# Kernel tuning notes

Measured on AMD Instinct MI355X. Metric: run time of the kernel, lower is better.

## Reference

```python
import jax, jax.numpy as jnp
import numpy as np
import math

B, S, D, H = 8, 1024, 512, 8
DH = D // H
SCALE_BASE = 512


def _xpos(x, downscale):
    # x: [B, H, S, DH]; xpos rotary with exponential scale (jamie-stirling RetNet impl)
    s = x.shape[-2]
    d = x.shape[-1]
    half = d // 2
    sv = (jnp.arange(0, d, 2, dtype=jnp.float32) + 0.4 * d) / (1.4 * d)      # [half]
    power = jnp.arange(s, dtype=jnp.float32) / SCALE_BASE
    scale = sv[None, :] ** power[:, None]                                     # [s, half]
    inv_freq = 1.0 / (10000.0 ** (jnp.arange(half, dtype=jnp.float32) / half))
    ang = jnp.arange(s, dtype=jnp.float32)[:, None] * inv_freq[None, :]       # [s, half]
    if downscale:
        scale = 1.0 / scale
    sin = jnp.repeat(jnp.sin(ang) * scale, 2, axis=-1)                        # [s, d]
    cos = jnp.repeat(jnp.cos(ang) * scale, 2, axis=-1)
    rot = jnp.stack((-x[..., 1::2], x[..., ::2]), axis=-1).reshape(x.shape)   # rotate_every_two
    return x * cos + rot * sin


def setup_inputs() -> dict:
    key = jax.random.key(0)
    ks = jax.random.split(key, 7)
    X = jax.random.normal(ks[0], (B, S, D), dtype=jnp.float32)
    # per-head projections stacked: torch init randn/hidden_size
    W_Q = jax.random.normal(ks[1], (H, D, DH), dtype=jnp.float32) / D
    W_K = jax.random.normal(ks[2], (H, D, DH), dtype=jnp.float32) / D
    W_V = jax.random.normal(ks[3], (H, D, DH), dtype=jnp.float32) / D
    W_G = jax.random.normal(ks[4], (D, D), dtype=jnp.float32) / D
    W_O = jax.random.normal(ks[5], (D, D), dtype=jnp.float32) / D
    gn_weight = jnp.ones((D,), dtype=jnp.float32)
    gn_bias = jnp.zeros((D,), dtype=jnp.float32)
    return {"X": X, "W_Q": W_Q, "W_K": W_K, "W_V": W_V, "W_G": W_G,
            "W_O": W_O, "gn_weight": gn_weight, "gn_bias": gn_bias}


def reference(X, W_Q, W_K, W_V, W_G, W_O, gn_weight, gn_bias):
    b, s, _ = X.shape
    # per-head decay gammas and symmetric (non-causal) decay matrix D
    gammas = 1.0 - jnp.exp(jnp.linspace(math.log(1.0 / 32), math.log(1.0 / 512), H)).astype(jnp.float32)
    n = jnp.arange(s)
    Dmat = gammas[:, None, None] ** jnp.abs(n[:, None] - n[None, :]).astype(jnp.float32)  # [H,s,s]
    Q = _xpos(jnp.einsum('bsd,hde->bhse', X, W_Q), False)
    K = _xpos(jnp.einsum('bsd,hde->bhse', X, W_K), True)
    V = jnp.einsum('bsd,hde->bhse', X, W_V)
    scores = jnp.einsum('bhse,bhte->bhst', Q, K)
    p = jax.nn.softmax(scores, axis=-1) * Dmat[None]          # decay-weighted softmax
    Y = jnp.einsum('bhst,bhte->bhse', p, V)                    # [b,H,s,DH]
    Y = jnp.moveaxis(Y, 1, 2).reshape(b, s, H * DH)            # concat heads -> [b,s,D]
    # GroupNorm(H groups) over flattened rows [b*s, D]
    Yg = Y.reshape(-1, H, DH)
    mu = Yg.mean(axis=-1, keepdims=True)
    var = Yg.var(axis=-1, keepdims=True)
    Yn = ((Yg - mu) * jax.lax.rsqrt(var + 1e-5)).reshape(-1, H * DH)
    Yn = (Yn * gn_weight + gn_bias).reshape(b, s, H * DH)
    G = X @ W_G
    swish = G * jax.nn.sigmoid(G)
    return (swish * Yn) @ W_O
```

## Files before the change

kernel.cpp:

```cpp
#include <hip/hip_runtime.h>
#include <math.h>

#define B_ 8
#define S_ 1024
#define D_ 512
#define H_ 8
#define DH_ 64
#define M_ (B_*S_)

typedef __attribute__((ext_vector_type(8))) short short8;
typedef __attribute__((ext_vector_type(4))) short s16x4;
typedef __attribute__((ext_vector_type(4))) float f32x4;
typedef __attribute__((ext_vector_type(4))) unsigned int u32x4;

__device__ inline void tsplit(float x, short& hs, short& ls) {
  unsigned u = __float_as_uint(x);
  hs = (short)(u >> 16);
  float r = x - __uint_as_float(u & 0xFFFF0000u);
  ls = (short)(__float_as_uint(r) >> 16);
}
__device__ inline void splitpack(f32x4 a, f32x4 b, short8& hh, short8& ll) {
  union { u32x4 u; short8 s; } H, L;
#pragma unroll
  for (int j = 0; j < 2; ++j) {
    unsigned u0 = __float_as_uint(a[2 * j]);
    unsigned u1 = __float_as_uint(a[2 * j + 1]);
    H.u[j] = (u0 >> 16) | (u1 & 0xFFFF0000u);
    float r0 = a[2 * j]     - __uint_as_float(u0 & 0xFFFF0000u);
    float r1 = a[2 * j + 1] - __uint_as_float(u1 & 0xFFFF0000u);
    L.u[j] = (__float_as_uint(r0) >> 16) | (__float_as_uint(r1) & 0xFFFF0000u);
    unsigned v0 = __float_as_uint(b[2 * j]);
    unsigned v1 = __float_as_uint(b[2 * j + 1]);
    H.u[2 + j] = (v0 >> 16) | (v1 & 0xFFFF0000u);
    float s0 = b[2 * j]     - __uint_as_float(v0 & 0xFFFF0000u);
    float s1 = b[2 * j + 1] - __uint_as_float(v1 & 0xFFFF0000u);
    L.u[2 + j] = (__float_as_uint(s0) >> 16) | (__float_as_uint(s1) & 0xFFFF0000u);
  }
  hh = H.s; ll = L.s;
}
__device__ inline f32x4 mfma16(short8 a, short8 b, f32x4 c) {
  return __builtin_amdgcn_mfma_f32_16x16x32_bf16(a, b, c, 0, 0, 0);
}
__device__ inline void gload_lds16(const void* g, void* l) {
  __builtin_amdgcn_global_load_lds(
      (const __attribute__((address_space(1))) void*)g,
      (__attribute__((address_space(3))) void*)l, 16, 0, 0);
}


__global__ void xpos_table_kernel(float* __restrict__ tab) {
  int idx = blockIdx.x * 256 + threadIdx.x;
  int s = idx >> 5, i = idx & 31;
  float sv = (2.0f * (float)i + 0.4f * 64.0f) / (1.4f * 64.0f);
  float p = (float)s / 512.0f;
  float scale = powf(sv, p);
  float inv_freq = powf(10000.0f, -((float)i / 32.0f));
  float ang = (float)s * inv_freq;
  float sn = sinf(ang), cs = cosf(ang);
  tab[idx]          = cs * scale;
  tab[32768 + idx]  = sn * scale;
  tab[65536 + idx]  = cs / scale;
  tab[98304 + idx]  = sn / scale;
}

__global__ __launch_bounds__(256) void xsplit_kernel(
    const float* __restrict__ X, short* __restrict__ Xh, short* __restrict__ Xl) {
  const int tid = threadIdx.x;
  const size_t tile = ((size_t)blockIdx.x * 16 + blockIdx.y) * 4096;
#pragma unroll
  for (int i = 0; i < 2; ++i) {
    int idx = tid + i * 256;
    int g = idx >> 6, sl = idx & 63;
    int m = blockIdx.x * 128 + g * 16 + (sl & 15);
    int k = blockIdx.y * 32 + (sl >> 4) * 8;
    const float* xp = X + (size_t)m * 512 + k;
    f32x4 a = *(const f32x4*)xp;
    f32x4 b = *(const f32x4*)(xp + 4);
    short8 hh, ll;
    splitpack(a, b, hh, ll);
    *(short8*)(Xh + tile + (size_t)idx * 8) = hh;
    *(short8*)(Xl + tile + (size_t)idx * 8) = ll;
  }
}

__global__ __launch_bounds__(256) void wprep_kernel(
    const float* __restrict__ Wq, const float* __restrict__ Wk,
    const float* __restrict__ Wv, const float* __restrict__ Wg,
    short* __restrict__ BTh, short* __restrict__ BTl, int gonly) {
  __shared__ float t[64][65];
  const int n0 = blockIdx.x * 64, k0 = blockIdx.y * 64;
  const int tid = threadIdx.x;
  const float* src;
  int ld;
  if (gonly) {
    src = Wg + (size_t)k0 * 512 + n0; ld = 512;
  } else {
    int w = n0 >> 9, nn = n0 & 511;
    if (w == 3) { src = Wg + (size_t)k0 * 512 + nn; ld = 512; }
    else {
      const float* W = (w == 0) ? Wq : ((w == 1) ? Wk : Wv);
      int h = nn >> 6;
      src = W + (size_t)h * D_ * DH_ + (size_t)k0 * 64; ld = 64;
    }
  }
#pragma unroll
  for (int i = 0; i < 4; ++i) {
    int idx = tid + i * 256;
    int kk = idx >> 4, nl4 = (idx & 15) * 4;
    float4 v = *(const float4*)(src + (size_t)kk * ld + nl4);
    t[kk][nl4] = v.x; t[kk][nl4 + 1] = v.y; t[kk][nl4 + 2] = v.z; t[kk][nl4 + 3] = v.w;
  }
  __syncthreads();
#pragma unroll
  for (int i = 0; i < 2; ++i) {
    int idx = tid + i * 256;
    int nl = idx >> 3, ck = idx & 7;
    short8 hh, ll;
#pragma unroll
    for (int j = 0; j < 8; ++j) {
      short h_, l_;
      tsplit(t[ck * 8 + j][nl], h_, l_);
      hh[j] = h_; ll[j] = l_;
    }
    const int n = n0 + nl, k = k0 + ck * 8;
    const size_t off = ((size_t)((n >> 7) * 16 + (k >> 5))) * 4096
                     + (size_t)((n >> 4) & 7) * 512
                     + (size_t)(((k >> 3) & 3) * 16 + (n & 15)) * 8;
    *(short8*)(BTh + off) = hh;
    *(short8*)(BTl + off) = ll;
  }
}

template<int NSUB, int FUSED>
__global__ __launch_bounds__(256, 2) void gemm_mfma_kernel(
    const short* __restrict__ Ah, const short* __restrict__ Al,
    const short* __restrict__ BTh, const short* __restrict__ BTl,
    const float* __restrict__ tab,
    short* __restrict__ QhO, short* __restrict__ QlO,
    short* __restrict__ KhO, short* __restrict__ KlO,
    short* __restrict__ VhT, short* __restrict__ VlT,
    float* __restrict__ G) {
  constexpr int NT = NSUB * 32;
  constexpr int BSZ = NT * 32;
  __shared__ __align__(16) short AsH[2 * 4096], AsL[2 * 4096];
  __shared__ __align__(16) short BsH[2 * BSZ], BsL[2 * BSZ];
  const int m0 = blockIdx.x * 128, by = blockIdx.y;
  const int tid = threadIdx.x, w = tid >> 6, lane = tid & 63;
  const int lx = lane & 15, quad = lane >> 4;
  const int wr = w >> 1, wc = w & 1;
  f32x4 acc[4][NSUB] = {};

  auto stage = [&](int bsel, int kt) {
    const size_t ta = ((size_t)blockIdx.x * 16 + kt) * 4096 + lane * 8;
    gload_lds16(Ah + ta + (size_t)w * 512,       &AsH[bsel * 4096 + w * 512]);
    gload_lds16(Ah + ta + (size_t)(w + 4) * 512, &AsH[bsel * 4096 + (w + 4) * 512]);
    gload_lds16(Al + ta + (size_t)w * 512,       &AsL[bsel * 4096 + w * 512]);
    gload_lds16(Al + ta + (size_t)(w + 4) * 512, &AsL[bsel * 4096 + (w + 4) * 512]);
    if constexpr (NSUB == 4) {
      const size_t tb = ((size_t)by * 16 + kt) * 4096 + lane * 8;
      gload_lds16(BTh + tb + (size_t)w * 512,       &BsH[bsel * BSZ + w * 512]);
      gload_lds16(BTh + tb + (size_t)(w + 4) * 512, &BsH[bsel * BSZ + (w + 4) * 512]);
      gload_lds16(BTl + tb + (size_t)w * 512,       &BsL[bsel * BSZ + w * 512]);
      gload_lds16(BTl + tb + (size_t)(w + 4) * 512, &BsL[bsel * BSZ + (w + 4) * 512]);
    } else {
      const size_t tb = ((size_t)(by >> 1) * 16 + kt) * 4096
                      + (size_t)(by & 1) * 2048 + lane * 8;
      const short* src = (w < 2) ? BTh : BTl;
      short* dst = (w < 2) ? &BsH[bsel * BSZ] : &BsL[bsel * BSZ];
      const int wq = (w & 1) * 2;
      gload_lds16(src + tb + (size_t)wq * 512,       dst + wq * 512);
      gload_lds16(src + tb + (size_t)(wq + 1) * 512, dst + (wq + 1) * 512);
    }
  };

  stage(0, 0);
  int cur = 0;
  for (int t = 0; t < 16; ++t) {
    asm volatile("s_waitcnt lgkmcnt(0)" ::: "memory");
    __builtin_amdgcn_s_barrier();
    asm volatile("" ::: "memory");
    if (t < 15) {
      stage(cur ^ 1, t + 1);
      if constexpr (NSUB == 4)
        asm volatile("s_waitcnt vmcnt(12)" ::: "memory");
      else
        asm volatile("s_waitcnt vmcnt(6)" ::: "memory");
    } else {
      asm volatile("s_waitcnt vmcnt(0)" ::: "memory");
    }
    __builtin_amdgcn_s_barrier();
    asm volatile("" ::: "memory");

    short8 fah[4], fal[4], fbh[NSUB], fbl[NSUB];
#pragma unroll
    for (int i = 0; i < 4; ++i) {
      fah[i] = *(const short8*)&AsH[cur * 4096 + (wr * 4 + i) * 512 + lane * 8];
      fal[i] = *(const short8*)&AsL[cur * 4096 + (wr * 4 + i) * 512 + lane * 8];
    }
#pragma unroll
    for (int i = 0; i < NSUB; ++i) {
      const int g = (NSUB == 4 ? wc * 4 : wc * 2) + i;
      fbh[i] = *(const short8*)&BsH[cur * BSZ + g * 512 + lane * 8];
      fbl[i] = *(const short8*)&BsL[cur * BSZ + g * 512 + lane * 8];
    }
#pragma unroll
    for (int ms = 0; ms < 4; ++ms)
#pragma unroll
      for (int ns = 0; ns < NSUB; ++ns) {
        f32x4 a = acc[ms][ns];
        a = mfma16(fah[ms], fbh[ns], a);
        a = mfma16(fal[ms], fbh[ns], a);
        a = mfma16(fah[ms], fbl[ns], a);
        acc[ms][ns] = a;
      }
    cur ^= 1;
  }
  if constexpr (FUSED) {
    const int w4 = by >> 2;
    const int ncb = (by & 3) * 128 + wc * 64;
    if (w4 < 2) {
      short* Ph = (w4 == 0) ? QhO : KhO;
      short* Pl = (w4 == 0) ? QlO : KlO;
      const float* ct = tab + (w4 ? 65536 : 0);
      const float* st = tab + (w4 ? 98304 : 32768);
#pragma unroll
      for (int ms = 0; ms < 4; ++ms) {
        const int m = m0 + wr * 64 + ms * 16 + quad * 4;
        const int b = m >> 10, sbase = m & 1023;
#pragma unroll
        for (int ns = 0; ns < 4; ++ns) {
          const int n = ncb + ns * 16 + lx;
          const int h = n >> 6, e = n & 63;
          const int i0 = e >> 1;
          const float sgn = (e & 1) ? 1.0f : -1.0f;
          short* ph = Ph + (((size_t)(b * 8 + h)) * 1024 + sbase) * 64 + e;
          short* pl = Pl + (((size_t)(b * 8 + h)) * 1024 + sbase) * 64 + e;
#pragma unroll
          for (int rg = 0; rg < 4; ++rg) {
            const int s = sbase + rg;
            float v = acc[ms][ns][rg];
            float vp = __shfl_xor(v, 1);
            float o = v * ct[s * 32 + i0] + sgn * vp * st[s * 32 + i0];
            short h_, l_;
            tsplit(o, h_, l_);
            ph[rg * 64] = h_;
            pl[rg * 64] = l_;
          }
        }
      }
    } else if (w4 == 2) {
#pragma unroll
      for (int ms = 0; ms < 4; ++ms) {
        const int m = m0 + wr * 64 + ms * 16 + quad * 4;
        const int b = m >> 10, s = m & 1023;
#pragma unroll
        for (int ns = 0; ns < 4; ++ns) {
          const int n = ncb + ns * 16 + lx;
          const int h = n >> 6, e = n & 63;
          s16x4 hh, ll;
#pragma unroll
          for (int rg = 0; rg < 4; ++rg) {
            short h_, l_;
            tsplit(acc[ms][ns][rg], h_, l_);
            hh[rg] = h_; ll[rg] = l_;
          }
          size_t off = (((size_t)(b * 8 + h)) * 64 + e) * 1024 + s;
          *(s16x4*)(VhT + off) = hh;
          *(s16x4*)(VlT + off) = ll;
        }
      }
    } else {
#pragma unroll
      for (int ms = 0; ms < 4; ++ms) {
        const int m = m0 + wr * 64 + ms * 16 + quad * 4;
#pragma unroll
        for (int ns = 0; ns < 4; ++ns) {
          const int n = ncb + ns * 16 + lx;
#pragma unroll
          for (int rg = 0; rg < 4; ++rg) G[(size_t)(m + rg) * 512 + n] = acc[ms][ns][rg];
        }
      }
    }
  } else {
#pragma unroll
    for (int ms = 0; ms < 4; ++ms) {
      const int m = m0 + wr * 64 + ms * 16 + quad * 4;
#pragma unroll
      for (int ns = 0; ns < NSUB; ++ns) {
        const int n = by * NT + wc * (NSUB * 16) + ns * 16 + lx;
#pragma unroll
        for (int rg = 0; rg < 4; ++rg) G[(size_t)(m + rg) * 512 + n] = acc[ms][ns][rg];
      }
    }
  }
}

__global__ __launch_bounds__(256, 2) void attn_mfma_kernel(
    const short* __restrict__ Qh, const short* __restrict__ Ql,
    const short* __restrict__ Kh, const short* __restrict__ Kl,
    const short* __restrict__ VhT, const short* __restrict__ VlT,
    const float* __restrict__ Gp,
    const float* __restrict__ gnw, const float* __restrict__ gnb,
    short* __restrict__ Zh, short* __restrict__ Zl) {
  __shared__ __align__(16) short KhS[4096];
  __shared__ __align__(16) short KlS[4096];
  __shared__ __align__(16) short VhS[4096];
  __shared__ __align__(16) short VlS[4096];
  __shared__ __align__(16) short PhS[4][2048];
  const int bh = blockIdx.x, s0 = blockIdx.y * 128;
  const int b = bh >> 3, h = bh & 7;
  const int tid = threadIdx.x;
  const int w = tid >> 6, lane = tid & 63;
  const int lx = lane & 15, quad = lane >> 4;
  const int s0w = s0 + w * 32;
  const float l0c = -3.4657359027997265f;
  const float l1c = -6.2383246250395075f;
  const float gamma = 1.0f - expf(l0c + (float)h * (l1c - l0c) / 7.0f);
  const float lg2g = log2f(gamma);
  const short* Qbh = Qh + (size_t)bh * S_ * DH_;
  const short* Qbl = Ql + (size_t)bh * S_ * DH_;
  const short* Kbh = Kh + (size_t)bh * S_ * DH_;
  const short* Kbl = Kl + (size_t)bh * S_ * DH_;
  const short* VbH = VhT + (size_t)bh * DH_ * S_;
  const short* VbL = VlT + (size_t)bh * DH_ * S_;

  float cl[4], cr[4], w4g[4], b4g[4];
#pragma unroll
  for (int ns = 0; ns < 4; ++ns) {
    cl[ns] = exp2f(lg2g * (float)(ns * 16 + lx));
    cr[ns] = exp2f(lg2g * (float)(63 - ns * 16 - lx));
    w4g[ns] = gnw[h * DH_ + ns * 16 + lx];
    b4g[ns] = gnb[h * DH_ + ns * 16 + lx];
  }

  short8 qfh[2][2], qfl[2][2];
#pragma unroll
  for (int ms = 0; ms < 2; ++ms)
#pragma unroll
    for (int kc = 0; kc < 2; ++kc) {
      size_t off = (size_t)(s0w + ms * 16 + lx) * DH_ + kc * 32 + quad * 8;
      qfh[ms][kc] = *(const short8*)(Qbh + off);
      qfl[ms][kc] = *(const short8*)(Qbl + off);
    }

  const int rA = tid >> 3, gsA = tid & 7;
  const int wA = gsA ^ (rA & 7);
  const int rB = rA + 32;
  short8 kAh, kAl, vAh, vAl, kBh, kBl, vBh, vBl;
#define ISSUE_KV(T0N) do {                                                   \
    kAh = *(const short8*)(Kbh + (size_t)((T0N) + rA) * 64 + gsA * 8);       \
    kAl = *(const short8*)(Kbl + (size_t)((T0N) + rA) * 64 + gsA * 8);       \
    vAh = *(const short8*)(VbH + (size_t)rA * 1024 + (T0N) + gsA * 8);       \
    vAl = *(const short8*)(VbL + (size_t)rA * 1024 + (T0N) + gsA * 8);       \
    kBh = *(const short8*)(Kbh + (size_t)((T0N) + rB) * 64 + gsA * 8);       \
    kBl = *(const short8*)(Kbl + (size_t)((T0N) + rB) * 64 + gsA * 8);       \
    vBh = *(const short8*)(VbH + (size_t)rB * 1024 + (T0N) + gsA * 8);       \
    vBl = *(const short8*)(VbL + (size_t)rB * 1024 + (T0N) + gsA * 8);       \
  } while (0)
#define WRITE_KV() do {                                                      \
    *(short8*)(KhS + rA * 64 + wA * 8) = kAh;                                \
    *(short8*)(KlS + rA * 64 + wA * 8) = kAl;                                \
    *(short8*)(VhS + rA * 64 + wA * 8) = vAh;                                \
    *(short8*)(VlS + rA * 64 + wA * 8) = vAl;                                \
    *(short8*)(KhS + rB * 64 + wA * 8) = kBh;                                \
    *(short8*)(KlS + rB * 64 + wA * 8) = kBl;                                \
    *(short8*)(VhS + rB * 64 + wA * 8) = vBh;                                \
    *(short8*)(VlS + rB * 64 + wA * 8) = vBl;                                \
  } while (0)

  f32x4 O[2][4] = {};
  float lsum[2][4] = {};

  ISSUE_KV(0);
  WRITE_KV();
  for (int t = 0; t < 16; ++t) {
    const int t0 = t * 64;
    __syncthreads();
    f32x4 acc[2][4];
#pragma unroll
    for (int ns = 0; ns < 4; ++ns) {
      const int rowk = ns * 16 + lx, rk = (rowk & 7) << 3;
      const short* Kc0 = &KhS[rowk * 64];
      const short* Kc1 = &KlS[rowk * 64];
      short8 kh0 = *(const short8*)(Kc0 + (((quad) << 3) ^ rk));
      short8 kh1 = *(const short8*)(Kc0 + (((4 | quad) << 3) ^ rk));
      short8 kl0 = *(const short8*)(Kc1 + (((quad) << 3) ^ rk));
      short8 kl1 = *(const short8*)(Kc1 + (((4 | quad) << 3) ^ rk));
#pragma unroll
      for (int ms = 0; ms < 2; ++ms) {
        f32x4 a = {};
        a = mfma16(qfh[ms][0], kh0, a);
        a = mfma16(qfl[ms][0], kh0, a);
        a = mfma16(qfh[ms][0], kl0, a);
        a = mfma16(qfh[ms][1], kh1, a);
        a = mfma16(qfl[ms][1], kh1, a);
        a = mfma16(qfh[ms][1], kl1, a);
        acc[ms][ns] = a;
      }
    }
    if (t < 15) ISSUE_KV(t0 + 64);
    const int cse = (t0 + 63 < s0w) ? 0 : ((t0 > s0w + 31) ? 1 : 2);
#pragma unroll
    for (int ms = 0; ms < 2; ++ms)
#pragma unroll
      for (int rg = 0; rg < 4; ++rg) {
        const int rloc = ms * 16 + quad * 4 + rg;
        const int srow = s0w + rloc;
        float pe[4], p[4];
#pragma unroll
        for (int ns = 0; ns < 4; ++ns) pe[ns] = __expf(acc[ms][ns][rg]);
        lsum[ms][rg] += (pe[0] + pe[1]) + (pe[2] + pe[3]);
        if (cse == 0) {
          float rf = exp2f(lg2g * (float)(srow - t0 - 63));
#pragma unroll
          for (int ns = 0; ns < 4; ++ns) p[ns] = pe[ns] * rf * cr[ns];
        } else if (cse == 1) {
          float rf = exp2f(lg2g * (float)(t0 - srow));
#pragma unroll
          for (int ns = 0; ns < 4; ++ns) p[ns] = pe[ns] * rf * cl[ns];
        } else {
#pragma unroll
          for (int ns = 0; ns < 4; ++ns)
            p[ns] = pe[ns] * exp2f(lg2g * fabsf((float)(srow - (t0 + ns * 16 + lx))));
        }
        const int r7s = rloc & 7;
        short* Pw = &PhS[w][rloc * 64 + (lx & 7)];
#pragma unroll
        for (int ns = 0; ns < 4; ++ns)
          Pw[(((ns * 2 + (lx >> 3)) ^ r7s) << 3)] =
              (short)((__float_as_uint(p[ns]) + 0x8000u) >> 16);
      }
    short8 pf[2][2];
#pragma unroll
    for (int ms = 0; ms < 2; ++ms) {
      const int rowp = ms * 16 + lx, rp = (rowp & 7) << 3;
#pragma unroll
      for (int kc = 0; kc < 2; ++kc)
        pf[ms][kc] = *(const short8*)&PhS[w][rowp * 64 + ((((kc * 4 + quad)) << 3) ^ rp)];
    }
#pragma unroll
    for (int ns = 0; ns < 4; ++ns) {
      const int rowv = ns * 16 + lx, rv = (rowv & 7) << 3;
      const short* Vc0 = &VhS[rowv * 64];
      const short* Vc1 = &VlS[rowv * 64];
      short8 vh0 = *(const short8*)(Vc0 + (((quad) << 3) ^ rv));
      short8 vh1 = *(const short8*)(Vc0 + (((4 | quad) << 3) ^ rv));
      short8 vl0 = *(const short8*)(Vc1 + (((quad) << 3) ^ rv));
      short8 vl1 = *(const short8*)(Vc1 + (((4 | quad) << 3) ^ rv));
#pragma unroll
      for (int ms = 0; ms < 2; ++ms) {
        f32x4 o = O[ms][ns];
        o = mfma16(pf[ms][0], vh0, o);
        o = mfma16(pf[ms][0], vl0, o);
        o = mfma16(pf[ms][1], vh1, o);
        o = mfma16(pf[ms][1], vl1, o);
        O[ms][ns] = o;
      }
    }
    __syncthreads();
    if (t < 15) WRITE_KV();
  }
#undef ISSUE_KV
#undef WRITE_KV
#pragma unroll
  for (int ms = 0; ms < 2; ++ms)
#pragma unroll
    for (int rg = 0; rg < 4; ++rg) {
      float s = lsum[ms][rg];
      s += __shfl_xor(s, 1);
      s += __shfl_xor(s, 2);
      s += __shfl_xor(s, 4);
      s += __shfl_xor(s, 8);
      const float inv = 1.0f / s;
      const int srow = s0w + ms * 16 + quad * 4 + rg;
      float y[4];
      float rs = 0.0f;
#pragma unroll
      for (int ns = 0; ns < 4; ++ns) { y[ns] = O[ms][ns][rg] * inv; rs += y[ns]; }
      rs += __shfl_xor(rs, 1);
      rs += __shfl_xor(rs, 2);
      rs += __shfl_xor(rs, 4);
      rs += __shfl_xor(rs, 8);
      const float mu = rs * (1.0f / 64.0f);
      float vv = 0.0f;
#pragma unroll
      for (int ns = 0; ns < 4; ++ns) { float d = y[ns] - mu; vv += d * d; }
      vv += __shfl_xor(vv, 1);
      vv += __shfl_xor(vv, 2);
      vv += __shfl_xor(vv, 4);
      vv += __shfl_xor(vv, 8);
      const float rstd = rsqrtf(vv * (1.0f / 64.0f) + 1e-5f);
      const size_t base = (size_t)(b * S_ + srow) * D_ + h * DH_;
      const int m = b * S_ + srow;
      const size_t zb = ((size_t)((m >> 7) * 16 + h * 2)) * 4096
                      + (size_t)((m >> 4) & 7) * 512 + (size_t)(m & 15) * 8;
#pragma unroll
      for (int ns = 0; ns < 4; ++ns) {
        float g = Gp[base + ns * 16 + lx];
        float sw = g / (1.0f + __expf(-g));
        float z = sw * ((y[ns] - mu) * rstd * w4g[ns] + b4g[ns]);
        short zh_, zl_;
        tsplit(z, zh_, zl_);
        const size_t off = zb + (size_t)(ns >> 1) * 4096
                         + (size_t)(((ns * 2 + (lx >> 3)) & 3) * 128) + (lx & 7);
        Zh[off] = zh_;
        Zl[off] = zl_;
      }
    }
}

extern "C" void kernel_launch(void* const* d_in, const int* in_sizes, int n_in,
                              void* d_out, int out_size, void* d_ws, size_t ws_size,
                              hipStream_t stream) {
  const float* X   = (const float*)d_in[0];
  const float* Wq  = (const float*)d_in[1];
  const float* Wk  = (const float*)d_in[2];
  const float* Wv  = (const float*)d_in[3];
  const float* Wg  = (const float*)d_in[4];
  const float* Wo  = (const float*)d_in[5];
  const float* gnw = (const float*)d_in[6];
  const float* gnb = (const float*)d_in[7];
  float* out = (float*)d_out;
  float* ws  = (float*)d_ws;
  const size_t NB = (size_t)M_ * D_;
  float* R0 = ws;
  float* R1 = ws + NB;
  float* R2 = ws + 2 * NB;
  float* R3 = ws + 3 * NB;
  float* tab = ws + 4 * NB;
  short* BTh = (short*)R3;
  short* BTl = BTh + (size_t)2048 * 512;
  short* Xh  = BTh + (size_t)2 * 2048 * 512;
  short* Xl  = (short*)(tab + 131072);
  short* Qh = (short*)R0;  short* Ql = Qh + NB;
  short* Kh = (short*)R1;  short* Kl = Kh + NB;
  short* VhT = (short*)R2; short* VlT = VhT + NB;
  short* Zh = (short*)R3;  short* Zl = Zh + NB;
  short* BToh = (short*)R1;
  short* BTol = BToh + (size_t)512 * 512;

  wprep_kernel<<<dim3(32, 8), 256, 0, stream>>>(Wq, Wk, Wv, Wg, BTh, BTl, 0);
  xpos_table_kernel<<<128, 256, 0, stream>>>(tab);
  xsplit_kernel<<<dim3(64, 16), 256, 0, stream>>>(X, Xh, Xl);
  gemm_mfma_kernel<4, 1><<<dim3(64, 16), 256, 0, stream>>>(
      Xh, Xl, BTh, BTl, tab, Qh, Ql, Kh, Kl, VhT, VlT, out);
  attn_mfma_kernel<<<dim3(64, 8), 256, 0, stream>>>(
      Qh, Ql, Kh, Kl, VhT, VlT, out, gnw, gnb, Zh, Zl);
  wprep_kernel<<<dim3(8, 8), 256, 0, stream>>>(nullptr, nullptr, nullptr, Wo, BToh, BTol, 1);
  gemm_mfma_kernel<2, 0><<<dim3(64, 8), 256, 0, stream>>>(
      Zh, Zl, BToh, BTol, nullptr, nullptr, nullptr, nullptr, nullptr,
      nullptr, nullptr, out);
}
```

Measured before the change: 216.4 us.

## Double-buffer K/V LDS tiles and raise wave priority around MFMA phases

K/V shared-memory tiles become double buffers so the next tile is written into the alternate buffer. That removes the second __syncthreads per iteration and leaves one barrier per tile. s_setprio also raises wave priority during the QK and PV MFMA loops to help interleave matrix work across waves. LDS use grows by 32KB per block (about 80KB total), which may lower occupancy below the launch_bounds target of 2 blocks per CU.

```diff
diff --git a/kernel.cpp b/kernel.cpp
--- a/kernel.cpp
+++ b/kernel.cpp
@@ -302,10 +302,10 @@
     const float* __restrict__ Gp,
     const float* __restrict__ gnw, const float* __restrict__ gnb,
     short* __restrict__ Zh, short* __restrict__ Zl) {
-  __shared__ __align__(16) short KhS[4096];
-  __shared__ __align__(16) short KlS[4096];
-  __shared__ __align__(16) short VhS[4096];
-  __shared__ __align__(16) short VlS[4096];
+  __shared__ __align__(16) short KhS[2][4096];
+  __shared__ __align__(16) short KlS[2][4096];
+  __shared__ __align__(16) short VhS[2][4096];
+  __shared__ __align__(16) short VlS[2][4096];
   __shared__ __align__(16) short PhS[4][2048];
   const int bh = blockIdx.x, s0 = blockIdx.y * 128;
   const int b = bh >> 3, h = bh & 7;
@@ -357,31 +357,33 @@
     vBh = *(const short8*)(VbH + (size_t)rB * 1024 + (T0N) + gsA * 8);       \
     vBl = *(const short8*)(VbL + (size_t)rB * 1024 + (T0N) + gsA * 8);       \
   } while (0)
-#define WRITE_KV() do {                                                      \
-    *(short8*)(KhS + rA * 64 + wA * 8) = kAh;                                \
-    *(short8*)(KlS + rA * 64 + wA * 8) = kAl;                                \
-    *(short8*)(VhS + rA * 64 + wA * 8) = vAh;                                \
-    *(short8*)(VlS + rA * 64 + wA * 8) = vAl;                                \
-    *(short8*)(KhS + rB * 64 + wA * 8) = kBh;                                \
-    *(short8*)(KlS + rB * 64 + wA * 8) = kBl;                                \
-    *(short8*)(VhS + rB * 64 + wA * 8) = vBh;                                \
-    *(short8*)(VlS + rB * 64 + wA * 8) = vBl;                                \
+#define WRITE_KV(BSEL) do {                                                  \
+    *(short8*)(&KhS[BSEL][rA * 64 + wA * 8]) = kAh;                          \
+    *(short8*)(&KlS[BSEL][rA * 64 + wA * 8]) = kAl;                          \
+    *(short8*)(&VhS[BSEL][rA * 64 + wA * 8]) = vAh;                          \
+    *(short8*)(&VlS[BSEL][rA * 64 + wA * 8]) = vAl;                          \
+    *(short8*)(&KhS[BSEL][rB * 64 + wA * 8]) = kBh;                          \
+    *(short8*)(&KlS[BSEL][rB * 64 + wA * 8]) = kBl;                          \
+    *(short8*)(&VhS[BSEL][rB * 64 + wA * 8]) = vBh;                          \
+    *(short8*)(&VlS[BSEL][rB * 64 + wA * 8]) = vBl;                          \
   } while (0)
 
   f32x4 O[2][4] = {};
   float lsum[2][4] = {};
 
   ISSUE_KV(0);
-  WRITE_KV();
+  WRITE_KV(0);
   for (int t = 0; t < 16; ++t) {
     const int t0 = t * 64;
+    const int cur = t & 1;
     __syncthreads();
     f32x4 acc[2][4];
+    __builtin_amdgcn_s_setprio(1);
 #pragma unroll
     for (int ns = 0; ns < 4; ++ns) {
       const int rowk = ns * 16 + lx, rk = (rowk & 7) << 3;
-      const short* Kc0 = &KhS[rowk * 64];
-      const short* Kc1 = &KlS[rowk * 64];
+      const short* Kc0 = &KhS[cur][rowk * 64];
+      const short* Kc1 = &KlS[cur][rowk * 64];
       short8 kh0 = *(const short8*)(Kc0 + (((quad) << 3) ^ rk));
       short8 kh1 = *(const short8*)(Kc0 + (((4 | quad) << 3) ^ rk));
       short8 kl0 = *(const short8*)(Kc1 + (((quad) << 3) ^ rk));
@@ -398,6 +400,7 @@
         acc[ms][ns] = a;
       }
     }
+    __builtin_amdgcn_s_setprio(0);
     if (t < 15) ISSUE_KV(t0 + 64);
     const int cse = (t0 + 63 < s0w) ? 0 : ((t0 > s0w + 31) ? 1 : 2);
 #pragma unroll
@@ -438,11 +441,12 @@
       for (int kc = 0; kc < 2; ++kc)
         pf[ms][kc] = *(const short8*)&PhS[w][rowp * 64 + ((((kc * 4 + quad)) << 3) ^ rp)];
     }
+    __builtin_amdgcn_s_setprio(1);
 #pragma unroll
     for (int ns = 0; ns < 4; ++ns) {
       const int rowv = ns * 16 + lx, rv = (rowv & 7) << 3;
-      const short* Vc0 = &VhS[rowv * 64];
-      const short* Vc1 = &VlS[rowv * 64];
+      const short* Vc0 = &VhS[cur][rowv * 64];
+      const short* Vc1 = &VlS[cur][rowv * 64];
       short8 vh0 = *(const short8*)(Vc0 + (((quad) << 3) ^ rv));
       short8 vh1 = *(const short8*)(Vc0 + (((4 | quad) << 3) ^ rv));
       short8 vl0 = *(const short8*)(Vc1 + (((quad) << 3) ^ rv));
@@ -457,8 +461,8 @@
         O[ms][ns] = o;
       }
     }
-    __syncthreads();
-    if (t < 15) WRITE_KV();
+    __builtin_amdgcn_s_setprio(0);
+    if (t < 15) WRITE_KV(cur ^ 1);
   }
 #undef ISSUE_KV
 #undef WRITE_KV
```

After: 217.0 us. No clear change (+0.3%).
